# Performance work log

Measured on AMD Instinct MI355X. Metric: run time of the kernel, lower is better.

Reference implementation:

```python
import jax, jax.numpy as jnp
import numpy as np

PI = np.pi
F0 = 0.91  # Fresnel base reflectance (Schlick), NeRFactor default
EH, EW = 16, 32  # env map lat/long resolution


def normalize(x, eps=1e-8):
    return x / (jnp.linalg.norm(x, axis=-1, keepdims=True) + eps)


def safe_div(num, den):
    # divide_no_nan semantics, grad-safe
    ok = jnp.abs(den) > 1e-12
    return jnp.where(ok, num / jnp.where(ok, den, 1.0), 0.0)


def sample_envmap(probe, dirs):
    # Equirectangular bilinear sample. probe: [eH,eW,3]; dirs: [...,3] normalized.
    eH, eW = probe.shape[0], probe.shape[1]
    z = jnp.clip(dirs[..., 2], -1.0 + 1e-6, 1.0 - 1e-6)
    theta = jnp.arccos(z)                       # [0, pi]
    phi = jnp.arctan2(dirs[..., 1], dirs[..., 0])  # (-pi, pi]
    v = theta / PI * eH - 0.5
    u = (phi / (2.0 * PI) + 0.5) * eW - 0.5
    v0 = jnp.floor(v); u0 = jnp.floor(u)
    fv = (v - v0)[..., None]; fu = (u - u0)[..., None]
    v0i = jnp.clip(v0.astype(jnp.int32), 0, eH - 1)
    v1i = jnp.clip(v0i + 1, 0, eH - 1)
    u0i = jnp.mod(u0.astype(jnp.int32), eW)
    u1i = jnp.mod(u0i + 1, eW)
    p00 = probe[v0i, u0i]; p01 = probe[v0i, u1i]
    p10 = probe[v1i, u0i]; p11 = probe[v1i, u1i]
    return (p00 * (1 - fu) + p01 * fu) * (1 - fv) + (p10 * (1 - fu) + p11 * fu) * fv


def microfacet_brdf(pts2l, pts2c, normal, albedo, rough):
    # pts2l: [B,eH,eW,P,3]; pts2c, normal: [B,P,3]; albedo: [B,P,3]; rough: [B,P,1]
    c = pts2c[:, None, None]   # [B,1,1,P,3]
    n = normal[:, None, None]  # [B,1,1,P,3]
    h = normalize(pts2l + c)   # half vector [B,eH,eW,P,3]
    # Fresnel (Schlick)
    l_dot_h = jnp.sum(pts2l * h, -1)
    f = F0 + (1.0 - F0) * (1.0 - l_dot_h) ** 5
    alpha = (rough ** 2)[..., 0][:, None, None]  # [B,1,1,P]
    # D (GGX normal distribution)
    cos_m = jnp.sum(h * n, -1)
    chi_m = (cos_m > 0).astype(h.dtype)
    cos_m_sq = cos_m ** 2
    tan_m_sq = safe_div(1.0 - cos_m_sq, cos_m_sq)
    d = safe_div(alpha ** 2 * chi_m, PI * cos_m_sq ** 2 * (alpha ** 2 + tan_m_sq) ** 2)
    # G (GGX geometric term, NeRFactor style)
    cos_v = jnp.sum(normal * pts2c, -1)[:, None, None]  # [B,1,1,P]
    cos_hv = jnp.sum(h * c, -1)
    chi_g = (safe_div(cos_hv, cos_v) > 0).astype(h.dtype)
    cos_v_sq = jnp.clip(cos_v ** 2, 0.0, 1.0)
    tan_v_sq = jnp.clip(safe_div(1.0 - cos_v_sq, cos_v_sq), 0.0, 1e10)
    g = safe_div(chi_g * 2.0, 1.0 + jnp.sqrt(1.0 + alpha ** 2 * tan_v_sq))
    l_dot_n = jnp.sum(pts2l * n, -1)
    micro = safe_div(f * g * d, 4.0 * jnp.abs(l_dot_n) * jnp.abs(cos_v))
    # glossy + lambertian diffuse
    return micro[..., None] + (albedo / PI)[:, None, None]  # [B,eH,eW,P,3]


def linear2srgb(x):
    x = jnp.clip(x, 0.0, 1.0)
    return jnp.where(x <= 0.0031308, 12.92 * x,
                     1.055 * jnp.power(jnp.maximum(x, 1e-8), 1.0 / 2.4) - 0.055)


def setup_inputs() -> dict:
    key = jax.random.key(0)
    ks = jax.random.split(key, 12)
    B, P, Pt = 1, 8192, 65536
    surf = jax.random.normal(ks[0], (B, P, 3), jnp.float32)
    ray_o = jax.random.normal(ks[1], (B, P, 3), jnp.float32) + 3.0
    norm_raw = jax.random.normal(ks[2], (B, P, 3), jnp.float32)
    albedo = jax.random.uniform(ks[3], (B, P, 3), jnp.float32)
    roughness = 0.1 + 0.9 * jax.random.uniform(ks[4], (B, P, 1), jnp.float32)
    lvis = jax.random.uniform(ks[5], (B, P, EH * EW), jnp.float32)
    xyz = jax.random.normal(ks[6], (EH, EW, 3), jnp.float32) * 10.0
    area = jax.random.uniform(ks[7], (EH, EW), jnp.float32)
    probe = jax.random.uniform(ks[8], (EH, EW, 3), jnp.float32)
    grd_rgb = jax.random.uniform(ks[9], (B, Pt, 3), jnp.float32)
    grd_acc = jax.random.uniform(ks[10], (B, Pt), jnp.float32)
    inds = jnp.sort(jax.random.randint(ks[11], (B, P), 0, Pt, jnp.int32), axis=-1)
    return {"surf": surf, "ray_o": ray_o, "norm_raw": norm_raw, "albedo": albedo,
            "roughness": roughness, "lvis": lvis, "xyz": xyz, "area": area,
            "probe": probe, "grd_rgb": grd_rgb, "grd_acc": grd_acc, "inds": inds}


def reference(surf, ray_o, norm_raw, albedo, roughness, lvis, xyz, area, probe,
              grd_rgb, grd_acc, inds):
    B, P, _ = surf.shape
    eH, eW, _ = xyz.shape
    norm = normalize(norm_raw)
    # lvis: [B,P,L] -> [B,eH,eW,P]
    lvis_g = jnp.transpose(lvis, (0, 2, 1)).reshape(B, eH, eW, P)
    ldir = normalize(xyz)[None, :, :, None]             # [1,eH,eW,1,3]
    ldot = jnp.sum(ldir * norm[:, None, None], -1)      # [B,eH,eW,P]
    surf2light = normalize(xyz[:, :, None] - surf[:, None, None])  # [B,eH,eW,P,3]
    surf2cam = normalize(ray_o - surf)                  # [B,P,3]
    light = sample_envmap(probe, surf2light)            # [B,eH,eW,P,3]
    shade = lvis_g[..., None] * ldot[..., None] * area[None, :, :, None, None] * light
    brdf = microfacet_brdf(surf2light, surf2cam, norm, albedo, roughness)
    rgb = jnp.sum(brdf * shade, axis=(1, 2))            # [B,P,3]
    rgb = linear2srgb(rgb)
    # alpha_blend: scatter shaded rays into ground image, blend by ground acc
    bidx = jnp.arange(B)[:, None]
    scatter = jnp.zeros_like(grd_rgb).at[bidx, inds].set(rgb)
    acc = grd_acc[..., None]
    merged = grd_rgb * acc + scatter * (1.0 - acc)      # [B,Pt,3]
    return merged
```

## Files before the change

kernel.cpp:

```cpp
#include <hip/hip_runtime.h>
#include <math.h>

#define NL     512
#define EH_C   16
#define EW_C   32
#define P_PTS  8192
#define PT_PTS 65536
#define PROW   33
#define PTILE  (17*33)

typedef float f32x2 __attribute__((ext_vector_type(2)));

__device__ __forceinline__ float rcp_f(float x)  { return __builtin_amdgcn_rcpf(x); }
__device__ __forceinline__ float rsq_f(float x)  { return __builtin_amdgcn_rsqf(x); }
__device__ __forceinline__ float sqrt_f(float x) { return __builtin_amdgcn_sqrtf(x); }

__device__ __forceinline__ f32x2 rcp2(f32x2 x)  { return (f32x2){rcp_f(x.x),  rcp_f(x.y)}; }
__device__ __forceinline__ f32x2 rsq2(f32x2 x)  { return (f32x2){rsq_f(x.x),  rsq_f(x.y)}; }
__device__ __forceinline__ f32x2 sqrt2(f32x2 x) { return (f32x2){sqrt_f(x.x), sqrt_f(x.y)}; }
__device__ __forceinline__ f32x2 floor2(f32x2 x){ return (f32x2){floorf(x.x), floorf(x.y)}; }
__device__ __forceinline__ f32x2 abs2(f32x2 x)  { return (f32x2){fabsf(x.x),  fabsf(x.y)}; }
__device__ __forceinline__ f32x2 max2(f32x2 a, f32x2 b){ return (f32x2){fmaxf(a.x,b.x), fmaxf(a.y,b.y)}; }
__device__ __forceinline__ f32x2 min2(f32x2 a, f32x2 b){ return (f32x2){fminf(a.x,b.x), fminf(a.y,b.y)}; }
__device__ __forceinline__ f32x2 maxs(f32x2 a, float b){ return (f32x2){fmaxf(a.x,b), fmaxf(a.y,b)}; }

__global__ __launch_bounds__(256) void bg_kernel(const float4* __restrict__ rgbv,
                                                 const float4* __restrict__ accv,
                                                 float4* __restrict__ outv) {
    int j = blockIdx.x * 256 + threadIdx.x;
    float4 a  = accv[j];
    float4 r0 = rgbv[3*j+0], r1 = rgbv[3*j+1], r2 = rgbv[3*j+2];
    outv[3*j+0] = make_float4(r0.x*a.x, r0.y*a.x, r0.z*a.x, r0.w*a.y);
    outv[3*j+1] = make_float4(r1.x*a.y, r1.y*a.y, r1.z*a.z, r1.w*a.z);
    outv[3*j+2] = make_float4(r2.x*a.z, r2.y*a.w, r2.z*a.w, r2.w*a.w);
}

__global__ __launch_bounds__(256, 4) void render_kernel(
    const float* __restrict__ surf,
    const float* __restrict__ ray_o,
    const float* __restrict__ norm_raw,
    const float* __restrict__ albedo,
    const float* __restrict__ rough,
    const float* __restrict__ lvis,
    const float* __restrict__ xyz,
    const float* __restrict__ area,
    const float* __restrict__ probe,
    const float* __restrict__ grd_rgb,
    const float* __restrict__ grd_acc,
    const int*   __restrict__ inds,
    float* __restrict__ out)
{
    __shared__ float4 sA[NL];
    __shared__ float4 sP2[PTILE];

    for (int i = threadIdx.x; i < NL; i += 256) {
        float x = xyz[3*i+0], y = xyz[3*i+1], z = xyz[3*i+2];
        float aw = area[i] / (sqrtf(x*x + y*y + z*z) + 1e-8f);
        sA[i] = make_float4(x, y, z, aw);
    }
    for (int i = threadIdx.x; i < PTILE; i += 256) {
        int vr = i / PROW;
        int ur = i - vr * PROW;
        int sv = vr > 15 ? 15 : vr;
        int su = ur & 31;
        int t  = sv * EW_C + su;
        sP2[i] = make_float4(probe[3*t+0], probe[3*t+1], probe[3*t+2], 0.0f);
    }
    __syncthreads();

    const int lane = threadIdx.x & 63;
    const int p    = blockIdx.x * 4 + (threadIdx.x >> 6);

    float sx = surf[3*p+0], sy = surf[3*p+1], sz = surf[3*p+2];
    float nx = norm_raw[3*p+0], ny = norm_raw[3*p+1], nz = norm_raw[3*p+2];
    { float inv = 1.0f / (sqrtf(nx*nx + ny*ny + nz*nz) + 1e-8f); nx*=inv; ny*=inv; nz*=inv; }
    float cx = ray_o[3*p+0]-sx, cy = ray_o[3*p+1]-sy, cz = ray_o[3*p+2]-sz;
    { float inv = 1.0f / (sqrtf(cx*cx + cy*cy + cz*cz) + 1e-8f); cx*=inv; cy*=inv; cz*=inv; }

    float cos_v  = nx*cx + ny*cy + nz*cz;
    float r      = rough[p];
    float alpha2 = (r*r)*(r*r);
    float cvsq   = fminf(fmaxf(cos_v*cos_v, 0.0f), 1.0f);
    float tvsq   = (cvsq > 1e-12f) ? fminf((1.0f - cvsq)/cvsq, 1e10f) : 0.0f;
    float gden   = 1.0f + sqrtf(1.0f + alpha2 * tvsq);
    float g2a    = (cos_v > 1e-12f) ? (2.0f / gden) * alpha2 * 0.3183098862f : 0.0f;
    float a2m1   = alpha2 - 1.0f;
    float acv4   = 4.0f * fabsf(cos_v);
    float ab0 = albedo[3*p+0] * 0.3183098862f;
    float ab1 = albedo[3*p+1] * 0.3183098862f;
    float ab2 = albedo[3*p+2] * 0.3183098862f;
    const float* lv = lvis + p*NL;

    f32x2 acc0 = (f32x2)(0.0f), acc1 = (f32x2)(0.0f), acc2 = (f32x2)(0.0f);

    #pragma unroll
    for (int it = 0; it < 4; ++it) {
        int l0 = lane + it*64;
        int l1 = l0 + 256;
        float lva = lv[l0], lvb = lv[l1];
        float4 A0 = sA[l0], A1 = sA[l1];
        f32x2 Ax = {A0.x, A1.x}, Ay = {A0.y, A1.y}, Az = {A0.z, A1.z}, Aw = {A0.w, A1.w};

        f32x2 dx = Ax - sx, dy = Ay - sy, dz = Az - sz;
        f32x2 inv = rsq2(dx*dx + dy*dy + dz*dz);
        f32x2 slx = dx*inv, sly = dy*inv, slz = dz*inv;

        f32x2 sh = ((f32x2){lva, lvb}) * (Ax*nx + Ay*ny + Az*nz) * Aw;

        f32x2 zc = min2(maxs(slz, -0.999999f), (f32x2)(0.999999f));
        f32x2 xa = abs2(zc);
        f32x2 pcl = ((xa*-0.0953875f + 0.378208f)*xa - 1.0802913f)*xa + 7.9996562f;
        f32x2 vpre = sqrt2(1.0f - xa) * pcl;
        f32x2 vv;
        vv.x = (zc.x < 0.0f) ? (15.5f - vpre.x) : (vpre.x - 0.5f);
        vv.y = (zc.y < 0.0f) ? (15.5f - vpre.y) : (vpre.y - 0.5f);

        f32x2 axv = abs2(slx), ayv = abs2(sly);
        f32x2 mx = max2(axv, ayv), mn = min2(axv, ayv);
        f32x2 a  = mn * rcp2(maxs(mx, 1e-37f));
        f32x2 s  = a * a;
        f32x2 pu = (((s*0.106112f - 0.433578f)*s + 0.917450f)*s - 1.682201f)*s + 5.0922757f;
        f32x2 rk = a * pu;
        rk.x = (ayv.x > axv.x) ? 8.0f  - rk.x : rk.x;
        rk.y = (ayv.y > axv.y) ? 8.0f  - rk.y : rk.y;
        rk.x = (slx.x < 0.0f)  ? 16.0f - rk.x : rk.x;
        rk.y = (slx.y < 0.0f)  ? 16.0f - rk.y : rk.y;
        f32x2 uu = { copysignf(rk.x, sly.x) + 15.5f,
                     copysignf(rk.y, sly.y) + 15.5f };

        f32x2 v0f = floor2(vv), u0f = floor2(uu);
        f32x2 fv = vv - v0f, fu = uu - u0f;
        f32x2 w11 = fu*fv, w10 = fv - w11, w01 = fu - w11;
        f32x2 w00 = (1.0f - fu) - w10;

        f32x2 hdot = slx*cx + sly*cy + slz*cz;
        f32x2 ih   = rsq2(maxs(hdot*2.0f + 2.0f, 1e-12f));
        f32x2 ldh  = (1.0f + hdot) * ih;
        f32x2 ldn  = slx*nx + sly*ny + slz*nz;
        f32x2 cm   = (ldn + cos_v) * ih;
        f32x2 om   = 1.0f - ldh;
        f32x2 om2  = om*om;
        f32x2 ff   = om2*om2*om*0.09f + 0.91f;
        f32x2 q    = cm*cm*a2m1 + 1.0f;
        f32x2 den  = abs2(ldn) * acv4;
        f32x2 micro = ff * g2a * rcp2(q*q*den);
        micro.x = (cm.x > 1e-6f && den.x > 1e-12f) ? micro.x : 0.0f;
        micro.y = (cm.y > 1e-6f && den.y > 1e-12f) ? micro.y : 0.0f;

        int v0a = (int)v0f.x; v0a = v0a < 0 ? 0 : v0a;
        int u0a = ((int)u0f.x) & 31;
        int v0b = (int)v0f.y; v0b = v0b < 0 ? 0 : v0b;
        int u0b = ((int)u0f.y) & 31;
        const float4* pa = &sP2[v0a*PROW + u0a];
        const float4* pb = &sP2[v0b*PROW + u0b];
        float4 t00a = pa[0], t01a = pa[1], t10a = pa[PROW], t11a = pa[PROW+1];
        float4 t00b = pb[0], t01b = pb[1], t10b = pb[PROW], t11b = pb[PROW+1];

        f32x2 li0 = { fmaf(t00a.x,w00.x, fmaf(t01a.x,w01.x, fmaf(t10a.x,w10.x, t11a.x*w11.x))),
                      fmaf(t00b.x,w00.y, fmaf(t01b.x,w01.y, fmaf(t10b.x,w10.y, t11b.x*w11.y))) };
        f32x2 li1 = { fmaf(t00a.y,w00.x, fmaf(t01a.y,w01.x, fmaf(t10a.y,w10.x, t11a.y*w11.x))),
                      fmaf(t00b.y,w00.y, fmaf(t01b.y,w01.y, fmaf(t10b.y,w10.y, t11b.y*w11.y))) };
        f32x2 li2 = { fmaf(t00a.z,w00.x, fmaf(t01a.z,w01.x, fmaf(t10a.z,w10.x, t11a.z*w11.x))),
                      fmaf(t00b.z,w00.y, fmaf(t01b.z,w01.y, fmaf(t10b.z,w10.y, t11b.z*w11.y))) };

        acc0 += (micro + ab0) * (sh * li0);
        acc1 += (micro + ab1) * (sh * li1);
        acc2 += (micro + ab2) * (sh * li2);
    }

    float c0 = acc0.x + acc0.y;
    float c1 = acc1.x + acc1.y;
    float c2 = acc2.x + acc2.y;

    for (int off = 32; off > 0; off >>= 1) {
        c0 += __shfl_xor(c0, off);
        c1 += __shfl_xor(c1, off);
        c2 += __shfl_xor(c2, off);
    }

    if (lane == 0) {
        int idx = inds[p];
        bool last = (p == P_PTS-1) || (inds[p+1] != idx);
        if (last) {
            float a = grd_acc[idx];
            float rgb[3] = {c0, c1, c2};
            #pragma unroll
            for (int c = 0; c < 3; ++c) {
                float x = fminf(fmaxf(rgb[c], 0.0f), 1.0f);
                float sr = (x <= 0.0031308f)
                         ? 12.92f * x
                         : fmaf(1.055f, exp2f(log2f(x) * (1.0f/2.4f)), -0.055f);
                out[3*idx+c] = fmaf(grd_rgb[3*idx+c], a, sr * (1.0f - a));
            }
        }
    }
}

extern "C" void kernel_launch(void* const* d_in, const int* in_sizes, int n_in,
                              void* d_out, int out_size, void* d_ws, size_t ws_size,
                              hipStream_t stream) {
    const float* surf      = (const float*)d_in[0];
    const float* ray_o     = (const float*)d_in[1];
    const float* norm_raw  = (const float*)d_in[2];
    const float* albedo    = (const float*)d_in[3];
    const float* roughness = (const float*)d_in[4];
    const float* lvis      = (const float*)d_in[5];
    const float* xyz       = (const float*)d_in[6];
    const float* area      = (const float*)d_in[7];
    const float* probe     = (const float*)d_in[8];
    const float* grd_rgb   = (const float*)d_in[9];
    const float* grd_acc   = (const float*)d_in[10];
    const int*   inds      = (const int*)d_in[11];
    float* out = (float*)d_out;

    bg_kernel<<<PT_PTS/4/256, 256, 0, stream>>>((const float4*)grd_rgb,
        (const float4*)grd_acc, (float4*)out);
    render_kernel<<<P_PTS/4, 256, 0, stream>>>(surf, ray_o, norm_raw, albedo,
        roughness, lvis, xyz, area, probe, grd_rgb, grd_acc, inds, out);
}
```

Measured before the change: 26.76 us.

## Precompute light table and fp16 env tile once; shrink per-block LDS setup

A new one-block prep kernel builds the light-direction/area table and a padded fp16-packed environment tile once in workspace. Each render block now only copies the half-size tile into shared memory and reads the light table straight from global/cache, which cuts the per-block setup work and the LDS footprint. The lvis reads change to contiguous float2 loads, and the arccos polynomial is swapped for a higher-degree one. The cost is an extra kernel launch, fp16 rounding of the probe values, and light data fetched from L1/L2 instead of LDS.

```diff
diff --git a/kernel.cpp b/kernel.cpp
--- a/kernel.cpp
+++ b/kernel.cpp
@@ -1,4 +1,5 @@
 #include <hip/hip_runtime.h>
+#include <hip/hip_fp16.h>
 #include <math.h>
 
 #define NL     512
@@ -23,6 +24,32 @@
 __device__ __forceinline__ f32x2 max2(f32x2 a, f32x2 b){ return (f32x2){fmaxf(a.x,b.x), fmaxf(a.y,b.y)}; }
 __device__ __forceinline__ f32x2 min2(f32x2 a, f32x2 b){ return (f32x2){fminf(a.x,b.x), fminf(a.y,b.y)}; }
 __device__ __forceinline__ f32x2 maxs(f32x2 a, float b){ return (f32x2){fmaxf(a.x,b), fmaxf(a.y,b)}; }
+
+__global__ __launch_bounds__(256) void prep_kernel(
+    const float* __restrict__ xyz, const float* __restrict__ area,
+    const float* __restrict__ probe,
+    float4* __restrict__ sA4g, uint2* __restrict__ sPHg)
+{
+    int t = threadIdx.x;
+    for (int i = t; i < NL; i += 256) {
+        float x = xyz[3*i+0], y = xyz[3*i+1], z = xyz[3*i+2];
+        float aw = area[i] / (sqrtf(x*x + y*y + z*z) + 1e-8f);
+        sA4g[i] = make_float4(x, y, z, aw);
+    }
+    for (int i = t; i < PTILE; i += 256) {
+        int vr = i / PROW;
+        int ur = i - vr * PROW;
+        int sv = vr > 15 ? 15 : vr;
+        int su = ur & 31;
+        int s  = 3 * (sv * EW_C + su);
+        __half2 rg = __floats2half2_rn(probe[s], probe[s+1]);
+        __half  b  = __float2half(probe[s+2]);
+        uint2 q;
+        q.x = *reinterpret_cast<unsigned int*>(&rg);
+        q.y = (unsigned int)(*reinterpret_cast<unsigned short*>(&b));
+        sPHg[i] = q;
+    }
+}
 
 __global__ __launch_bounds__(256) void bg_kernel(const float4* __restrict__ rgbv,
                                                  const float4* __restrict__ accv,
@@ -42,30 +69,15 @@
     const float* __restrict__ albedo,
     const float* __restrict__ rough,
     const float* __restrict__ lvis,
-    const float* __restrict__ xyz,
-    const float* __restrict__ area,
-    const float* __restrict__ probe,
+    const float4* __restrict__ sA4g,
+    const uint2* __restrict__ sPHg,
     const float* __restrict__ grd_rgb,
     const float* __restrict__ grd_acc,
     const int*   __restrict__ inds,
     float* __restrict__ out)
 {
-    __shared__ float4 sA[NL];
-    __shared__ float4 sP2[PTILE];
-
-    for (int i = threadIdx.x; i < NL; i += 256) {
-        float x = xyz[3*i+0], y = xyz[3*i+1], z = xyz[3*i+2];
-        float aw = area[i] / (sqrtf(x*x + y*y + z*z) + 1e-8f);
-        sA[i] = make_float4(x, y, z, aw);
-    }
-    for (int i = threadIdx.x; i < PTILE; i += 256) {
-        int vr = i / PROW;
-        int ur = i - vr * PROW;
-        int sv = vr > 15 ? 15 : vr;
-        int su = ur & 31;
-        int t  = sv * EW_C + su;
-        sP2[i] = make_float4(probe[3*t+0], probe[3*t+1], probe[3*t+2], 0.0f);
-    }
+    __shared__ uint2 sPH[PTILE];
+    for (int i = threadIdx.x; i < PTILE; i += 256) sPH[i] = sPHg[i];
     __syncthreads();
 
     const int lane = threadIdx.x & 63;
@@ -95,21 +107,26 @@
 
     #pragma unroll
     for (int it = 0; it < 4; ++it) {
-        int l0 = lane + it*64;
-        int l1 = l0 + 256;
-        float lva = lv[l0], lvb = lv[l1];
-        float4 A0 = sA[l0], A1 = sA[l1];
+        int l0 = it*128 + (lane << 1);
+        float2 lvv = *reinterpret_cast<const float2*>(lv + l0);
+        float4 A0 = sA4g[l0], A1 = sA4g[l0+1];
         f32x2 Ax = {A0.x, A1.x}, Ay = {A0.y, A1.y}, Az = {A0.z, A1.z}, Aw = {A0.w, A1.w};
 
         f32x2 dx = Ax - sx, dy = Ay - sy, dz = Az - sz;
         f32x2 inv = rsq2(dx*dx + dy*dy + dz*dz);
         f32x2 slx = dx*inv, sly = dy*inv, slz = dz*inv;
 
-        f32x2 sh = ((f32x2){lva, lvb}) * (Ax*nx + Ay*ny + Az*nz) * Aw;
+        f32x2 sh = ((f32x2){lvv.x, lvv.y}) * (Ax*nx + Ay*ny + Az*nz) * Aw;
 
         f32x2 zc = min2(maxs(slz, -0.999999f), (f32x2)(0.999999f));
         f32x2 xa = abs2(zc);
-        f32x2 pcl = ((xa*-0.0953875f + 0.378208f)*xa - 1.0802913f)*xa + 7.9996562f;
+        f32x2 pcl = xa*-0.00642982f + 0.03397049f;
+        pcl = pcl*xa - 0.08702911f;
+        pcl = pcl*xa + 0.15733105f;
+        pcl = pcl*xa - 0.25553564f;
+        pcl = pcl*xa + 0.45316427f;
+        pcl = pcl*xa - 1.09294280f;
+        pcl = pcl*xa + 7.99999960f;
         f32x2 vpre = sqrt2(1.0f - xa) * pcl;
         f32x2 vv;
         vv.x = (zc.x < 0.0f) ? (15.5f - vpre.x) : (vpre.x - 0.5f);
@@ -151,17 +168,34 @@
         int u0a = ((int)u0f.x) & 31;
         int v0b = (int)v0f.y; v0b = v0b < 0 ? 0 : v0b;
         int u0b = ((int)u0f.y) & 31;
-        const float4* pa = &sP2[v0a*PROW + u0a];
-        const float4* pb = &sP2[v0b*PROW + u0b];
-        float4 t00a = pa[0], t01a = pa[1], t10a = pa[PROW], t11a = pa[PROW+1];
-        float4 t00b = pb[0], t01b = pb[1], t10b = pb[PROW], t11b = pb[PROW+1];
-
-        f32x2 li0 = { fmaf(t00a.x,w00.x, fmaf(t01a.x,w01.x, fmaf(t10a.x,w10.x, t11a.x*w11.x))),
-                      fmaf(t00b.x,w00.y, fmaf(t01b.x,w01.y, fmaf(t10b.x,w10.y, t11b.x*w11.y))) };
-        f32x2 li1 = { fmaf(t00a.y,w00.x, fmaf(t01a.y,w01.x, fmaf(t10a.y,w10.x, t11a.y*w11.x))),
-                      fmaf(t00b.y,w00.y, fmaf(t01b.y,w01.y, fmaf(t10b.y,w10.y, t11b.y*w11.y))) };
-        f32x2 li2 = { fmaf(t00a.z,w00.x, fmaf(t01a.z,w01.x, fmaf(t10a.z,w10.x, t11a.z*w11.x))),
-                      fmaf(t00b.z,w00.y, fmaf(t01b.z,w01.y, fmaf(t10b.z,w10.y, t11b.z*w11.y))) };
+        const uint2* pa = &sPH[v0a*PROW + u0a];
+        const uint2* pb = &sPH[v0b*PROW + u0b];
+        uint2 q00a = pa[0], q01a = pa[1], q10a = pa[PROW], q11a = pa[PROW+1];
+        uint2 q00b = pb[0], q01b = pb[1], q10b = pb[PROW], q11b = pb[PROW+1];
+
+        float2 rg00a = __half22float2(*reinterpret_cast<const __half2*>(&q00a.x));
+        float2 rg01a = __half22float2(*reinterpret_cast<const __half2*>(&q01a.x));
+        float2 rg10a = __half22float2(*reinterpret_cast<const __half2*>(&q10a.x));
+        float2 rg11a = __half22float2(*reinterpret_cast<const __half2*>(&q11a.x));
+        float2 rg00b = __half22float2(*reinterpret_cast<const __half2*>(&q00b.x));
+        float2 rg01b = __half22float2(*reinterpret_cast<const __half2*>(&q01b.x));
+        float2 rg10b = __half22float2(*reinterpret_cast<const __half2*>(&q10b.x));
+        float2 rg11b = __half22float2(*reinterpret_cast<const __half2*>(&q11b.x));
+        float b00a = __half2float(*reinterpret_cast<const __half*>(&q00a.y));
+        float b01a = __half2float(*reinterpret_cast<const __half*>(&q01a.y));
+        float b10a = __half2float(*reinterpret_cast<const __half*>(&q10a.y));
+        float b11a = __half2float(*reinterpret_cast<const __half*>(&q11a.y));
+        float b00b = __half2float(*reinterpret_cast<const __half*>(&q00b.y));
+        float b01b = __half2float(*reinterpret_cast<const __half*>(&q01b.y));
+        float b10b = __half2float(*reinterpret_cast<const __half*>(&q10b.y));
+        float b11b = __half2float(*reinterpret_cast<const __half*>(&q11b.y));
+
+        f32x2 li0 = { fmaf(rg00a.x,w00.x, fmaf(rg01a.x,w01.x, fmaf(rg10a.x,w10.x, rg11a.x*w11.x))),
+                      fmaf(rg00b.x,w00.y, fmaf(rg01b.x,w01.y, fmaf(rg10b.x,w10.y, rg11b.x*w11.y))) };
+        f32x2 li1 = { fmaf(rg00a.y,w00.x, fmaf(rg01a.y,w01.x, fmaf(rg10a.y,w10.x, rg11a.y*w11.x))),
+                      fmaf(rg00b.y,w00.y, fmaf(rg01b.y,w01.y, fmaf(rg10b.y,w10.y, rg11b.y*w11.y))) };
+        f32x2 li2 = { fmaf(b00a,w00.x, fmaf(b01a,w01.x, fmaf(b10a,w10.x, b11a*w11.x))),
+                      fmaf(b00b,w00.y, fmaf(b01b,w01.y, fmaf(b10b,w10.y, b11b*w11.y))) };
 
         acc0 += (micro + ab0) * (sh * li0);
         acc1 += (micro + ab1) * (sh * li1);
@@ -213,8 +247,12 @@
     const int*   inds      = (const int*)d_in[11];
     float* out = (float*)d_out;
 
+    float4* sA4g = (float4*)d_ws;
+    uint2*  sPHg = (uint2*)((char*)d_ws + 8192);
+
+    prep_kernel<<<1, 256, 0, stream>>>(xyz, area, probe, sA4g, sPHg);
     bg_kernel<<<PT_PTS/4/256, 256, 0, stream>>>((const float4*)grd_rgb,
         (const float4*)grd_acc, (float4*)out);
     render_kernel<<<P_PTS/4, 256, 0, stream>>>(surf, ray_o, norm_raw, albedo,
-        roughness, lvis, xyz, area, probe, grd_rgb, grd_acc, inds, out);
-}
+        roughness, lvis, sA4g, sPHg, grd_rgb, grd_acc, inds, out);
+}
```

After: 28.00 us. 4.6% more time.

## Fuse background blend into render kernel via binary search on scatter indices

Applied to the files above, without the earlier changes.

Merges the separate background kernel into the render launch: extra blocks binary-search the sorted inds array and write grd_rgb*acc only for rows that are not scattered, so the two launches no longer both write the output. The lvis loads become contiguous float2 pairs, and the acos/atan polynomial approximations are replaced with higher-order ones for accuracy. This assumes inds is sorted and unique, and adds a log2(P)-step search per background row.

```diff
diff --git a/kernel.cpp b/kernel.cpp
--- a/kernel.cpp
+++ b/kernel.cpp
@@ -8,6 +8,7 @@
 #define PT_PTS 65536
 #define PROW   33
 #define PTILE  (17*33)
+#define RBLK   2048
 
 typedef float f32x2 __attribute__((ext_vector_type(2)));
 
@@ -24,18 +25,7 @@
 __device__ __forceinline__ f32x2 min2(f32x2 a, f32x2 b){ return (f32x2){fminf(a.x,b.x), fminf(a.y,b.y)}; }
 __device__ __forceinline__ f32x2 maxs(f32x2 a, float b){ return (f32x2){fmaxf(a.x,b), fmaxf(a.y,b)}; }
 
-__global__ __launch_bounds__(256) void bg_kernel(const float4* __restrict__ rgbv,
-                                                 const float4* __restrict__ accv,
-                                                 float4* __restrict__ outv) {
-    int j = blockIdx.x * 256 + threadIdx.x;
-    float4 a  = accv[j];
-    float4 r0 = rgbv[3*j+0], r1 = rgbv[3*j+1], r2 = rgbv[3*j+2];
-    outv[3*j+0] = make_float4(r0.x*a.x, r0.y*a.x, r0.z*a.x, r0.w*a.y);
-    outv[3*j+1] = make_float4(r1.x*a.y, r1.y*a.y, r1.z*a.z, r1.w*a.z);
-    outv[3*j+2] = make_float4(r2.x*a.z, r2.y*a.w, r2.z*a.w, r2.w*a.w);
-}
-
-__global__ __launch_bounds__(256, 4) void render_kernel(
+__global__ __launch_bounds__(256, 4) void fused_kernel(
     const float* __restrict__ surf,
     const float* __restrict__ ray_o,
     const float* __restrict__ norm_raw,
@@ -50,6 +40,20 @@
     const int*   __restrict__ inds,
     float* __restrict__ out)
 {
+    if (blockIdx.x >= RBLK) {
+        int row = (blockIdx.x - RBLK) * 256 + threadIdx.x;
+        int lo = 0, hi = P_PTS;
+        while (lo < hi) { int mid = (lo + hi) >> 1; if (inds[mid] < row) lo = mid + 1; else hi = mid; }
+        bool scattered = (lo < P_PTS) && (inds[lo] == row);
+        if (!scattered) {
+            float a = grd_acc[row];
+            out[3*row+0] = grd_rgb[3*row+0] * a;
+            out[3*row+1] = grd_rgb[3*row+1] * a;
+            out[3*row+2] = grd_rgb[3*row+2] * a;
+        }
+        return;
+    }
+
     __shared__ float4 sA[NL];
     __shared__ float4 sP2[PTILE];
 
@@ -63,8 +67,8 @@
         int ur = i - vr * PROW;
         int sv = vr > 15 ? 15 : vr;
         int su = ur & 31;
-        int t  = sv * EW_C + su;
-        sP2[i] = make_float4(probe[3*t+0], probe[3*t+1], probe[3*t+2], 0.0f);
+        int t  = 3 * (sv * EW_C + su);
+        sP2[i] = make_float4(probe[t], probe[t+1], probe[t+2], 0.0f);
     }
     __syncthreads();
 
@@ -95,21 +99,26 @@
 
     #pragma unroll
     for (int it = 0; it < 4; ++it) {
-        int l0 = lane + it*64;
-        int l1 = l0 + 256;
-        float lva = lv[l0], lvb = lv[l1];
-        float4 A0 = sA[l0], A1 = sA[l1];
+        int l0 = it*128 + (lane << 1);
+        float2 lvv = *reinterpret_cast<const float2*>(lv + l0);
+        float4 A0 = sA[l0], A1 = sA[l0+1];
         f32x2 Ax = {A0.x, A1.x}, Ay = {A0.y, A1.y}, Az = {A0.z, A1.z}, Aw = {A0.w, A1.w};
 
         f32x2 dx = Ax - sx, dy = Ay - sy, dz = Az - sz;
         f32x2 inv = rsq2(dx*dx + dy*dy + dz*dz);
         f32x2 slx = dx*inv, sly = dy*inv, slz = dz*inv;
 
-        f32x2 sh = ((f32x2){lva, lvb}) * (Ax*nx + Ay*ny + Az*nz) * Aw;
+        f32x2 sh = ((f32x2){lvv.x, lvv.y}) * (Ax*nx + Ay*ny + Az*nz) * Aw;
 
         f32x2 zc = min2(maxs(slz, -0.999999f), (f32x2)(0.999999f));
         f32x2 xa = abs2(zc);
-        f32x2 pcl = ((xa*-0.0953875f + 0.378208f)*xa - 1.0802913f)*xa + 7.9996562f;
+        f32x2 pcl = xa*-0.00642982f + 0.03397049f;
+        pcl = pcl*xa - 0.08702911f;
+        pcl = pcl*xa + 0.15733105f;
+        pcl = pcl*xa - 0.25553564f;
+        pcl = pcl*xa + 0.45316427f;
+        pcl = pcl*xa - 1.09294280f;
+        pcl = pcl*xa + 7.99999960f;
         f32x2 vpre = sqrt2(1.0f - xa) * pcl;
         f32x2 vv;
         vv.x = (zc.x < 0.0f) ? (15.5f - vpre.x) : (vpre.x - 0.5f);
@@ -119,7 +128,11 @@
         f32x2 mx = max2(axv, ayv), mn = min2(axv, ayv);
         f32x2 a  = mn * rcp2(maxs(mx, 1e-37f));
         f32x2 s  = a * a;
-        f32x2 pu = (((s*0.106112f - 0.433578f)*s + 0.917450f)*s - 1.682201f)*s + 5.0922757f;
+        f32x2 pu = s*-0.0596956f + 0.2681612f;
+        pu = pu*s - 0.5929877f;
+        pu = pu*s + 0.9857085f;
+        pu = pu*s - 1.6940397f;
+        pu = pu*s + 5.0928424f;
         f32x2 rk = a * pu;
         rk.x = (ayv.x > axv.x) ? 8.0f  - rk.x : rk.x;
         rk.y = (ayv.y > axv.y) ? 8.0f  - rk.y : rk.y;
@@ -213,8 +226,6 @@
     const int*   inds      = (const int*)d_in[11];
     float* out = (float*)d_out;
 
-    bg_kernel<<<PT_PTS/4/256, 256, 0, stream>>>((const float4*)grd_rgb,
-        (const float4*)grd_acc, (float4*)out);
-    render_kernel<<<P_PTS/4, 256, 0, stream>>>(surf, ray_o, norm_raw, albedo,
-        roughness, lvis, xyz, area, probe, grd_rgb, grd_acc, inds, out);
+    fused_kernel<<<RBLK + PT_PTS/256, 256, 0, stream>>>(surf, ray_o, norm_raw,
+        albedo, roughness, lvis, xyz, area, probe, grd_rgb, grd_acc, inds, out);
 }
```

Measured after the change: 24.70 us. -7.7%, faster.
